# Optimization experiments

Hardware: AMD Instinct MI355X
Metric: run time of the kernel (lower is better)

The kernel has to match this reference:

```python
import jax, jax.numpy as jnp
import numpy as np

K = 2        # top-k experts
ALPHA = 0.01  # load-balance loss weight
BETA = 0.1    # z-router loss weight

B, T, D, E = 4, 4096, 2048, 64


def setup_inputs() -> dict:
    key = jax.random.key(0)
    kx, kw = jax.random.split(key)
    x = jax.random.normal(kx, (B, T, D), dtype=jnp.float32)
    W = jax.random.normal(kw, (D, E), dtype=jnp.float32) * (1.0 / np.sqrt(D))
    b = jnp.zeros((E,), dtype=jnp.float32)
    return {"x": x, "W": W, "b": b}


def reference(x, W, b):
    # Router logits and softmax: [B, T, E]
    logits = jnp.einsum("btd,de->bte", x, W) + b
    scores = jax.nn.softmax(logits, axis=-1)

    # Top-k selection and renormalized combine weights: [B, T, K]
    topk_vals, topk_idx = jax.lax.top_k(scores, K)
    combine = topk_vals / jnp.sum(topk_vals, axis=-1, keepdims=True)

    # Load-balance loss (Fedus et al. 2022): f_e = fraction of tokens whose
    # max score is expert e; P_e = mean prob mass on expert e.
    is_max = (scores == jnp.max(scores, axis=-1, keepdims=True)).astype(jnp.float32)
    f = jnp.mean(is_max, axis=(0, 1))   # [E]
    P = jnp.mean(scores, axis=(0, 1))   # [E]
    balance_loss = ALPHA * jnp.mean(f * P)

    # Z-router loss; faithfully applied to post-softmax scores as in source.
    lse = jax.nn.logsumexp(scores, axis=-1)  # [B, T]
    z_loss = BETA * jnp.mean(lse ** 2)

    return topk_idx, combine, balance_loss, z_loss
```

## Files before the change

### kernel.cpp

```cpp
#include <hip/hip_runtime.h>
#include <math.h>

#define NTOK 16384
#define DDIM 2048
#define NEXP 64
#define MT   16
#define KCH  128
#define NCH  (DDIM / KCH)

#define ACC_N  129
#define WF_OFF 256
#define VSTRIDE ((size_t)4 * 64 * 64 * 8)

typedef __attribute__((ext_vector_type(8))) short short8_t;
typedef __attribute__((ext_vector_type(4))) float f32x4;

__device__ __forceinline__ unsigned short f2bf(float f) {
    unsigned int u = __float_as_uint(f);
    u += 0x7fffu + ((u >> 16) & 1u);
    return (unsigned short)(u >> 16);
}
__device__ __forceinline__ float bf2f(unsigned short s) {
    return __uint_as_float(((unsigned int)s) << 16);
}

__global__ __launch_bounds__(256) void prep(
    const float* __restrict__ W, float* __restrict__ ws)
{
    const int i = blockIdx.x * 256 + threadIdx.x;
    if (blockIdx.x == 0 && threadIdx.x < ACC_N) ws[threadIdx.x] = 0.0f;
    const int k = i >> 6, e = i & 63;
    const float v = W[i];
    unsigned short h = f2bf(v);
    float r1 = v - bf2f(h);
    unsigned short m = f2bf(r1);
    unsigned short l = f2bf(r1 - bf2f(m));
    unsigned short* wf = (unsigned short*)(ws + WF_OFF);
    const int g = e >> 4, ks = k >> 5;
    const int lane = (((k >> 3) & 3) << 4) | (e & 15);
    const int j = k & 7;
    const size_t base = ((((size_t)g * 64) + ks) * 64 + lane) * 8 + j;
    wf[base] = h;
    wf[VSTRIDE + base] = m;
    wf[2 * VSTRIDE + base] = l;
}

__global__ __launch_bounds__(256, 4) void gate_fused(
    const float* __restrict__ x, const unsigned short* __restrict__ wf,
    const float* __restrict__ bias, float* __restrict__ out,
    float* __restrict__ acc_g)
{
    __shared__ __align__(16) unsigned short xh[2][MT * KCH];
    __shared__ __align__(16) unsigned short xm_[2][MT * KCH];
    __shared__ __align__(16) unsigned short xl_[2][MT * KCH];
    __shared__ float logits[MT][68];
    __shared__ int   f_loc[NEXP];
    __shared__ float p_loc[NEXP];
    __shared__ float z_loc;

    const int tid  = threadIdx.x;
    const int tok0 = blockIdx.x * MT;
    const int lane = tid & 63;
    const int g    = __builtin_amdgcn_readfirstlane(tid >> 6);

    if (tid < NEXP) { f_loc[tid] = 0; p_loc[tid] = 0.0f; }
    if (tid == 0) z_loc = 0.0f;

    const int srow = tid >> 4;
    const int scg  = tid & 15;
    const float* xs = x + (size_t)(tok0 + srow) * DDIM + scg * 8;
    const int wbase = srow * KCH;
    const int s0 = (scg ^ (srow & 7)) * 8;

    const int arow  = lane & 15;
    const int akq   = lane >> 4;
    const int abase = arow * KCH;

    f32x4 acc = {0.0f, 0.0f, 0.0f, 0.0f};

    {
        float4 a0 = *(const float4*)(xs + 0);
        float4 a1 = *(const float4*)(xs + 4);
        float xv[8];
        *(float4*)&xv[0] = a0; *(float4*)&xv[4] = a1;
        unsigned short th[8], tm[8], tl[8];
        #pragma unroll
        for (int i = 0; i < 8; ++i) {
            float f = xv[i];
            th[i] = f2bf(f);
            float r = f - bf2f(th[i]);
            tm[i] = f2bf(r);
            tl[i] = f2bf(r - bf2f(tm[i]));
        }
        *(short8_t*)&xh[0][wbase + s0]  = *(short8_t*)&th[0];
        *(short8_t*)&xm_[0][wbase + s0] = *(short8_t*)&tm[0];
        *(short8_t*)&xl_[0][wbase + s0] = *(short8_t*)&tl[0];
    }
    float4 pv0 = *(const float4*)(xs + KCH + 0);
    float4 pv1 = *(const float4*)(xs + KCH + 4);

    #pragma unroll 1
    for (int c = 0; c < NCH; ++c) {
        __syncthreads();
        const int cb = c & 1, nb = cb ^ 1;

        const unsigned short* wb0 =
            wf + ((((size_t)g * 64) + c * 4) * 64 + lane) * 8;
        short8_t B[12];
        #pragma unroll
        for (int s = 0; s < 4; ++s) {
            const unsigned short* wb = wb0 + (size_t)s * 64 * 8;
            B[s * 3 + 0] = *(const short8_t*)&wb[0];
            B[s * 3 + 1] = *(const short8_t*)&wb[VSTRIDE];
            B[s * 3 + 2] = *(const short8_t*)&wb[2 * VSTRIDE];
        }

        if (c + 1 < NCH) {
            float xv[8];
            *(float4*)&xv[0] = pv0; *(float4*)&xv[4] = pv1;
            unsigned short th[8], tm[8], tl[8];
            #pragma unroll
            for (int i = 0; i < 8; ++i) {
                float f = xv[i];
                th[i] = f2bf(f);
                float r = f - bf2f(th[i]);
                tm[i] = f2bf(r);
                tl[i] = f2bf(r - bf2f(tm[i]));
            }
            *(short8_t*)&xh[nb][wbase + s0]  = *(short8_t*)&th[0];
            *(short8_t*)&xm_[nb][wbase + s0] = *(short8_t*)&tm[0];
            *(short8_t*)&xl_[nb][wbase + s0] = *(short8_t*)&tl[0];
            if (c + 2 < NCH) {
                const float* xn = xs + (c + 2) * KCH;
                pv0 = *(const float4*)(xn + 0);
                pv1 = *(const float4*)(xn + 4);
            }
        }

        #pragma unroll
        for (int s = 0; s < 4; ++s) {
            const int slot = (((s * 4 + akq) ^ (arow & 7))) * 8;
            short8_t ah = *(const short8_t*)&xh[cb][abase + slot];
            short8_t am = *(const short8_t*)&xm_[cb][abase + slot];
            short8_t al = *(const short8_t*)&xl_[cb][abase + slot];
            acc = __builtin_amdgcn_mfma_f32_16x16x32_bf16(ah, B[s*3+0], acc, 0, 0, 0);
            acc = __builtin_amdgcn_mfma_f32_16x16x32_bf16(ah, B[s*3+1], acc, 0, 0, 0);
            acc = __builtin_amdgcn_mfma_f32_16x16x32_bf16(am, B[s*3+0], acc, 0, 0, 0);
            acc = __builtin_amdgcn_mfma_f32_16x16x32_bf16(ah, B[s*3+2], acc, 0, 0, 0);
            acc = __builtin_amdgcn_mfma_f32_16x16x32_bf16(am, B[s*3+1], acc, 0, 0, 0);
            acc = __builtin_amdgcn_mfma_f32_16x16x32_bf16(al, B[s*3+0], acc, 0, 0, 0);
        }
    }

    #pragma unroll
    for (int r = 0; r < 4; ++r)
        logits[akq * 4 + r][g * 16 + arow] = acc[r];
    __syncthreads();

    const int tx = tid & 15;
    const int tg = tid >> 4;
    const int e0 = tx * 4;
    const int gt = tok0 + tg;

    float bb[4];
    *(float4*)bb = *(const float4*)&bias[e0];
    float l[4];
    {
        float4 lv = *(const float4*)&logits[tg][e0];
        l[0] = lv.x + bb[0]; l[1] = lv.y + bb[1];
        l[2] = lv.z + bb[2]; l[3] = lv.w + bb[3];
    }

    float v1 = l[0], v2 = -INFINITY;
    int   i1 = e0,   i2 = 0x7fffffff;
    #pragma unroll
    for (int j = 1; j < 4; ++j) {
        float v = l[j]; int e = e0 + j;
        if (v > v1)      { v2 = v1; i2 = i1; v1 = v; i1 = e; }
        else if (v > v2) { v2 = v;  i2 = e; }
    }
    #pragma unroll
    for (int off = 1; off < 16; off <<= 1) {
        float o1 = __shfl_xor(v1, off, 16); int oi1 = __shfl_xor(i1, off, 16);
        float o2 = __shfl_xor(v2, off, 16); int oi2 = __shfl_xor(i2, off, 16);
        if (o1 > v1 || (o1 == v1 && oi1 < i1)) {
            float cs = v1; int ci = i1;
            v1 = o1; i1 = oi1;
            if (cs > o2 || (cs == o2 && ci < oi2)) { v2 = cs; i2 = ci;  }
            else                                   { v2 = o2; i2 = oi2; }
        } else {
            if (o1 > v2 || (o1 == v2 && oi1 < i2)) { v2 = o1; i2 = oi1; }
        }
    }
    const float mx = v1;

    float sden[4], dsum = 0.0f;
    #pragma unroll
    for (int j = 0; j < 4; ++j) { sden[j] = __expf(l[j] - mx); dsum += sden[j]; }
    #pragma unroll
    for (int off = 1; off < 16; off <<= 1) dsum += __shfl_xor(dsum, off, 16);
    const float inv = 1.0f / dsum;

    float p[4], zsum = 0.0f;
    #pragma unroll
    for (int j = 0; j < 4; ++j) {
        p[j] = sden[j] * inv;
        zsum += __expf(p[j]);
    }
    #pragma unroll
    for (int off = 1; off < 16; off <<= 1) zsum += __shfl_xor(zsum, off, 16);

    float zacc = 0.0f;
    if (tx == 0) {
        const float s2 = __expf(v2 - mx);
        const float ci = 1.0f / (1.0f + s2);
        out[2 * gt]     = (float)i1;
        out[2 * gt + 1] = (float)i2;
        out[2 * NTOK + 2 * gt]     = ci;
        out[2 * NTOK + 2 * gt + 1] = s2 * ci;
        atomicAdd(&f_loc[i1], 1);
        float lse = __logf(zsum);
        zacc = lse * lse;
    }

    #pragma unroll
    for (int off = 1; off < 64; off <<= 1) zacc += __shfl_xor(zacc, off);
    if ((tid & 63) == 0) atomicAdd(&z_loc, zacc);

    #pragma unroll
    for (int j = 0; j < 4; ++j) {
        p[j] += __shfl_xor(p[j], 16);
        p[j] += __shfl_xor(p[j], 32);
    }
    if ((tid & 63) < 16) {
        #pragma unroll
        for (int j = 0; j < 4; ++j) atomicAdd(&p_loc[e0 + j], p[j]);
    }

    __syncthreads();
    if (tid < NEXP) {
        atomicAdd(&acc_g[64 + tid], p_loc[tid]);
        if (f_loc[tid]) atomicAdd(&acc_g[tid], (float)f_loc[tid]);
    }
    if (tid == 0) atomicAdd(&acc_g[128], z_loc);
}

__global__ void gate_finalize(const float* __restrict__ acc, float* __restrict__ out) {
    int e = threadIdx.x;
    float v = acc[e] * acc[64 + e];
    #pragma unroll
    for (int off = 32; off > 0; off >>= 1) v += __shfl_down(v, off);
    if (e == 0) {
        const float NT = (float)NTOK;
        out[2 * NTOK * 2]     = 0.01f * (v / (float)NEXP) / (NT * NT);
        out[2 * NTOK * 2 + 1] = 0.1f * acc[128] / NT;
    }
}

extern "C" void kernel_launch(void* const* d_in, const int* in_sizes, int n_in,
                              void* d_out, int out_size, void* d_ws, size_t ws_size,
                              hipStream_t stream) {
    const float* x    = (const float*)d_in[0];
    const float* W    = (const float*)d_in[1];
    const float* bias = (const float*)d_in[2];
    float* out = (float*)d_out;
    float* ws  = (float*)d_ws;
    const unsigned short* wfrag = (const unsigned short*)(ws + WF_OFF);

    prep<<<(DDIM * NEXP) / 256, 256, 0, stream>>>(W, ws);
    gate_fused<<<NTOK / MT, 256, 0, stream>>>(x, wfrag, bias, out, ws);
    gate_finalize<<<1, 64, 0, stream>>>(ws, out);
}
```

Measured before the change: 66.93 us.

## Split MFMA accumulator chains, stagger K-chunk order per block, raise priority

Replaces the single serial MFMA accumulator with three independent accumulators, so back-to-back MFMAs no longer wait on each other's results, and sums them at the end. Each block starts its K-chunk walk at a phase offset based on its block index, spreading concurrent W reads across different cache lines and channels. It also forces the W fragments to be materialised before the MFMA burst and raises wave priority around it. The reordered summation changes floating-point rounding slightly, which could flip near-tie top-k or argmax results.

Result: slower. 69.76 us (+4.2%).

```diff
diff --git a/kernel.cpp b/kernel.cpp
--- a/kernel.cpp
+++ b/kernel.cpp
@@ -62,6 +62,7 @@
     const int tok0 = blockIdx.x * MT;
     const int lane = tid & 63;
     const int g    = __builtin_amdgcn_readfirstlane(tid >> 6);
+    const int phase = (blockIdx.x & 3) * 4;
 
     if (tid < NEXP) { f_loc[tid] = 0; p_loc[tid] = 0.0f; }
     if (tid == 0) z_loc = 0.0f;
@@ -76,11 +77,14 @@
     const int akq   = lane >> 4;
     const int abase = arow * KCH;
 
-    f32x4 acc = {0.0f, 0.0f, 0.0f, 0.0f};
+    f32x4 acc0 = {0.f, 0.f, 0.f, 0.f};
+    f32x4 acc1 = {0.f, 0.f, 0.f, 0.f};
+    f32x4 acc2 = {0.f, 0.f, 0.f, 0.f};
 
     {
-        float4 a0 = *(const float4*)(xs + 0);
-        float4 a1 = *(const float4*)(xs + 4);
+        const float* x0 = xs + phase * KCH;
+        float4 a0 = *(const float4*)(x0 + 0);
+        float4 a1 = *(const float4*)(x0 + 4);
         float xv[8];
         *(float4*)&xv[0] = a0; *(float4*)&xv[4] = a1;
         unsigned short th[8], tm[8], tl[8];
@@ -96,16 +100,18 @@
         *(short8_t*)&xm_[0][wbase + s0] = *(short8_t*)&tm[0];
         *(short8_t*)&xl_[0][wbase + s0] = *(short8_t*)&tl[0];
     }
-    float4 pv0 = *(const float4*)(xs + KCH + 0);
-    float4 pv1 = *(const float4*)(xs + KCH + 4);
+    const float* xp1 = xs + ((phase + 1) & (NCH - 1)) * KCH;
+    float4 pv0 = *(const float4*)(xp1 + 0);
+    float4 pv1 = *(const float4*)(xp1 + 4);
 
     #pragma unroll 1
     for (int c = 0; c < NCH; ++c) {
         __syncthreads();
         const int cb = c & 1, nb = cb ^ 1;
+        const int actual = (phase + c) & (NCH - 1);
 
         const unsigned short* wb0 =
-            wf + ((((size_t)g * 64) + c * 4) * 64 + lane) * 8;
+            wf + ((((size_t)g * 64) + actual * 4) * 64 + lane) * 8;
         short8_t B[12];
         #pragma unroll
         for (int s = 0; s < 4; ++s) {
@@ -131,30 +137,36 @@
             *(short8_t*)&xm_[nb][wbase + s0] = *(short8_t*)&tm[0];
             *(short8_t*)&xl_[nb][wbase + s0] = *(short8_t*)&tl[0];
             if (c + 2 < NCH) {
-                const float* xn = xs + (c + 2) * KCH;
+                const float* xn = xs + ((phase + c + 2) & (NCH - 1)) * KCH;
                 pv0 = *(const float4*)(xn + 0);
                 pv1 = *(const float4*)(xn + 4);
             }
         }
 
+        #pragma unroll
+        for (int i = 0; i < 12; ++i)
+            asm volatile("" :: "v"(B[i]));
+
+        __builtin_amdgcn_s_setprio(1);
         #pragma unroll
         for (int s = 0; s < 4; ++s) {
             const int slot = (((s * 4 + akq) ^ (arow & 7))) * 8;
             short8_t ah = *(const short8_t*)&xh[cb][abase + slot];
             short8_t am = *(const short8_t*)&xm_[cb][abase + slot];
             short8_t al = *(const short8_t*)&xl_[cb][abase + slot];
-            acc = __builtin_amdgcn_mfma_f32_16x16x32_bf16(ah, B[s*3+0], acc, 0, 0, 0);
-            acc = __builtin_amdgcn_mfma_f32_16x16x32_bf16(ah, B[s*3+1], acc, 0, 0, 0);
-            acc = __builtin_amdgcn_mfma_f32_16x16x32_bf16(am, B[s*3+0], acc, 0, 0, 0);
-            acc = __builtin_amdgcn_mfma_f32_16x16x32_bf16(ah, B[s*3+2], acc, 0, 0, 0);
-            acc = __builtin_amdgcn_mfma_f32_16x16x32_bf16(am, B[s*3+1], acc, 0, 0, 0);
-            acc = __builtin_amdgcn_mfma_f32_16x16x32_bf16(al, B[s*3+0], acc, 0, 0, 0);
-        }
+            acc0 = __builtin_amdgcn_mfma_f32_16x16x32_bf16(ah, B[s*3+0], acc0, 0, 0, 0);
+            acc1 = __builtin_amdgcn_mfma_f32_16x16x32_bf16(ah, B[s*3+1], acc1, 0, 0, 0);
+            acc2 = __builtin_amdgcn_mfma_f32_16x16x32_bf16(am, B[s*3+1], acc2, 0, 0, 0);
+            acc0 = __builtin_amdgcn_mfma_f32_16x16x32_bf16(ah, B[s*3+2], acc0, 0, 0, 0);
+            acc1 = __builtin_amdgcn_mfma_f32_16x16x32_bf16(am, B[s*3+0], acc1, 0, 0, 0);
+            acc2 = __builtin_amdgcn_mfma_f32_16x16x32_bf16(al, B[s*3+0], acc2, 0, 0, 0);
+        }
+        __builtin_amdgcn_s_setprio(0);
     }
 
     #pragma unroll
     for (int r = 0; r < 4; ++r)
-        logits[akq * 4 + r][g * 16 + arow] = acc[r];
+        logits[akq * 4 + r][g * 16 + arow] = (acc0[r] + acc1[r]) + acc2[r];
     __syncthreads();
 
     const int tx = tid & 15;
```
